# Performance work log

Measured on AMD Instinct MI355X. Metric: run time of the kernel, lower is better.

Reference implementation:

```python
import jax, jax.numpy as jnp
import numpy as np
from jax import lax

# Norse default LIF/LI parameters with dt=0.001
DT_TAU_MEM = 0.1   # dt * tau_mem_inv (1/1e-2)
DT_TAU_SYN = 0.2   # dt * tau_syn_inv (1/5e-3)
V_TH = 0.5
ALPHA = 100.0      # SuperSpike surrogate slope (backward only)

@jax.custom_vjp
def spike(x):
    return (x > 0).astype(x.dtype)

def _spike_fwd(x):
    return (x > 0).astype(x.dtype), x

def _spike_bwd(x, g):
    # SuperSpike surrogate gradient: 1 / (alpha*|x| + 1)^2
    sg = 1.0 / (ALPHA * jnp.abs(x) + 1.0) ** 2
    return (g * sg,)

spike.defvjp(_spike_fwd, _spike_bwd)

def setup_inputs() -> dict:
    key = jax.random.key(0)
    k1, k2, k3 = jax.random.split(key, 3)
    T, B, C, H, W = 64, 512, 1, 28, 28
    IN, HID, OUT = 784, 2048, 10
    x = jax.random.normal(k1, (T, B, C, H, W), dtype=jnp.float32)
    # Kaiming-uniform-ish bias-free Linear weights, torch layout [out, in]
    w1 = jax.random.uniform(k2, (HID, IN), jnp.float32, -1.0, 1.0) / np.sqrt(IN)
    w_out = jax.random.uniform(k3, (OUT, HID), jnp.float32, -1.0, 1.0) / np.sqrt(HID)
    return {"x": x, "w1": w1, "w_out": w_out}

def reference(x, w1, w_out):
    T, B = x.shape[0], x.shape[1]
    HID, OUT = w1.shape[0], w_out.shape[0]
    xf = x.reshape(T, B, -1)  # [T, B, IN]

    def step(carry, xt):
        v1, i1, vo, io = carry
        cur = xt @ w1.T                       # fc1: [B, HID]
        # LIF: decay, threshold/spike/reset, then integrate new input current
        v1_dec = v1 + DT_TAU_MEM * (-v1 + i1)
        i1_dec = i1 * (1.0 - DT_TAU_SYN)
        z = spike(v1_dec - V_TH)
        v1_new = (1.0 - z) * v1_dec           # v_reset = 0
        i1_new = i1_dec + cur
        out_cur = z @ w_out.T                 # fc_out: [B, OUT]
        # LI readout: leaky integration (no spiking)
        vo_new = vo + DT_TAU_MEM * (-vo + io)
        io_new = io * (1.0 - DT_TAU_SYN) + out_cur
        return (v1_new, i1_new, vo_new, io_new), vo_new

    zh = jnp.zeros((B, HID), x.dtype)
    zo = jnp.zeros((B, OUT), x.dtype)
    _, voltages = lax.scan(step, (zh, zh, zo, zo), xf)  # [T, B, OUT]
    return jnp.max(voltages, axis=0)
```

## Files before the change

kernel.cpp:

```cpp
#include <hip/hip_runtime.h>
#include <cstdint>
#include <cstddef>

#define T_STEPS 64
#define BATCH 512
#define IN_F 784
#define NKT 25
#define HID 2048
#define OUT_F 10

#define DEC_V 0.9f
#define DEC_I 0.8f
#define DT_V 0.1f
#define V_TH 0.5f

typedef __attribute__((ext_vector_type(8))) _Float16 f16x8;
typedef __attribute__((ext_vector_type(4))) float f32x4;

__device__ __forceinline__ void load_lds16h(const _Float16* g, _Float16* l) {
  __builtin_amdgcn_global_load_lds(
      (const __attribute__((address_space(1))) void*)g,
      (__attribute__((address_space(3))) void*)l, 16, 0, 0);
}

__global__ __launch_bounds__(256)
void split_frag(const float* __restrict__ src, _Float16* __restrict__ hiT,
                _Float16* __restrict__ loT) {
  __shared__ float xr[16][804];
  const int mt = blockIdx.x;
  for (int i = threadIdx.x; i < 16 * IN_F; i += 256) {
    const int r = i / IN_F, c = i - r * IN_F;
    xr[r][c] = src[(size_t)(mt * 16 + r) * IN_F + c];
  }
  for (int i = threadIdx.x; i < 16 * 16; i += 256)
    xr[i >> 4][IN_F + (i & 15)] = 0.0f;
  __syncthreads();

  const int l = threadIdx.x & 63;
  const int g = threadIdx.x >> 6;
  const int r = l & 15, q = l >> 4;
  for (int kt = g; kt < NKT; kt += 4) {
    const float* s = &xr[r][kt * 32 + q * 8];
    f16x8 h, lo;
#pragma unroll
    for (int j = 0; j < 8; ++j) {
      const float v = s[j];
      const _Float16 hh = (_Float16)v;
      h[j] = hh;
      lo[j] = (_Float16)(v - (float)hh);
    }
    const size_t off = ((size_t)mt * NKT + kt) * 512 + l * 8;
    *(f16x8*)&hiT[off] = h;
    *(f16x8*)&loT[off] = lo;
  }
}

__global__ __launch_bounds__(256, 2)
void gemm_fc1(const _Float16* __restrict__ AhT, const _Float16* __restrict__ AlT,
              const _Float16* __restrict__ WhT, const _Float16* __restrict__ WlT,
              float* __restrict__ C) {
  __shared__ _Float16 __attribute__((aligned(16))) sAh[8 * 512];
  __shared__ _Float16 __attribute__((aligned(16))) sAl[8 * 512];
  __shared__ _Float16 __attribute__((aligned(16))) sWh[16 * 512];
  __shared__ _Float16 __attribute__((aligned(16))) sWl[16 * 512];

  const int tid = threadIdx.x;
  const int lane = tid & 63;
  const int wv = tid >> 6;
  const int bmT = blockIdx.y * 8;
  const int bnT = blockIdx.x * 16;

  const int wrT = (wv >> 1) * 4;
  const int wcT = (wv & 1) * 8;
  const int col = lane & 15;
  const int quad = lane >> 4;

  f32x4 acc[4][8] = {};

  for (int kt = 0; kt < NKT; ++kt) {
    __syncthreads();
#pragma unroll
    for (int j = 0; j < 2; ++j) {
      const int t = wv * 2 + j;
      const size_t go = ((size_t)(bmT + t) * NKT + kt) * 512 + lane * 8;
      load_lds16h(AhT + go, sAh + t * 512);
      load_lds16h(AlT + go, sAl + t * 512);
    }
#pragma unroll
    for (int j = 0; j < 4; ++j) {
      const int t = wv * 4 + j;
      const size_t go = ((size_t)(bnT + t) * NKT + kt) * 512 + lane * 8;
      load_lds16h(WhT + go, sWh + t * 512);
      load_lds16h(WlT + go, sWl + t * 512);
    }
    __syncthreads();

    f16x8 fah[4], fal[4];
#pragma unroll
    for (int i = 0; i < 4; ++i) {
      fah[i] = *(const f16x8*)&sAh[(wrT + i) * 512 + lane * 8];
      fal[i] = *(const f16x8*)&sAl[(wrT + i) * 512 + lane * 8];
    }
#pragma unroll
    for (int ni = 0; ni < 8; ++ni) {
      const f16x8 fwh = *(const f16x8*)&sWh[(wcT + ni) * 512 + lane * 8];
      const f16x8 fwl = *(const f16x8*)&sWl[(wcT + ni) * 512 + lane * 8];
#pragma unroll
      for (int mi = 0; mi < 4; ++mi) {
        acc[mi][ni] = __builtin_amdgcn_mfma_f32_16x16x32_f16(fah[mi], fwh, acc[mi][ni], 0, 0, 0);
        acc[mi][ni] = __builtin_amdgcn_mfma_f32_16x16x32_f16(fah[mi], fwl, acc[mi][ni], 0, 0, 0);
        acc[mi][ni] = __builtin_amdgcn_mfma_f32_16x16x32_f16(fal[mi], fwh, acc[mi][ni], 0, 0, 0);
      }
    }
  }

  const int rowb = blockIdx.y * 128 + (wv >> 1) * 64;
  const int colb = blockIdx.x * 256 + (wv & 1) * 128;
#pragma unroll
  for (int mi = 0; mi < 4; ++mi)
#pragma unroll
    for (int ni = 0; ni < 8; ++ni)
#pragma unroll
      for (int r = 0; r < 4; ++r)
        C[(size_t)(rowb + mi * 16 + quad * 4 + r) * HID + colb + ni * 16 + col] =
            acc[mi][ni][r];
}

__global__ __launch_bounds__(256)
void lif_out(const float* __restrict__ cur, const float* __restrict__ wo,
             float* __restrict__ v1, float* __restrict__ i1,
             float* __restrict__ outP, int tc, int t0) {
  __shared__ _Float16 zL[T_STEPS][264];
  __shared__ _Float16 wT[16][264];

  const int tid = threadIdx.x;
  const int hc = blockIdx.x;
  const int b = blockIdx.y;
  const int hb = hc * 256;

  for (int i = tid; i < 16 * 256; i += 256) {
    const int n = i >> 8, k = i & 255;
    wT[n][k] = (n < OUT_F) ? (_Float16)wo[(size_t)n * HID + hb + k] : (_Float16)0.f;
  }

  const int sidx = b * HID + hb + tid;
  float v = v1[sidx];
  float ci = i1[sidx];
#pragma unroll 4
  for (int t = 0; t < tc; ++t) {
    const float c = cur[(size_t)t * (BATCH * HID) + sidx];
    const float vd = DEC_V * v + DT_V * ci;
    const float z = (vd > V_TH) ? 1.0f : 0.0f;
    v = (1.0f - z) * vd;
    ci = DEC_I * ci + c;
    zL[t][tid] = (_Float16)z;
  }
  v1[sidx] = v;
  i1[sidx] = ci;
  __syncthreads();

  const int wv = tid >> 6;
  const int lane = tid & 63;
  const int col = lane & 15;
  const int quad = lane >> 4;
  f32x4 acc = {};
  const _Float16* za = &zL[wv * 16 + col][0];
  const _Float16* wb = &wT[col][0];
#pragma unroll
  for (int ks = 0; ks < 8; ++ks) {
    f16x8 a = *(const f16x8*)(za + ks * 32 + quad * 8);
    f16x8 bb = *(const f16x8*)(wb + ks * 32 + quad * 8);
    acc = __builtin_amdgcn_mfma_f32_16x16x32_f16(a, bb, acc, 0, 0, 0);
  }
  if (col < OUT_F) {
#pragma unroll
    for (int r = 0; r < 4; ++r) {
      const int t = wv * 16 + quad * 4 + r;
      if (t < tc)
        outP[(((size_t)hc * T_STEPS + (t0 + t)) * BATCH + b) * OUT_F + col] = acc[r];
    }
  }
}

__global__ __launch_bounds__(256)
void li_scan(const float* __restrict__ outP, float* __restrict__ out) {
  const int idx = blockIdx.x * 256 + threadIdx.x;
  if (idx >= BATCH * OUT_F) return;
  float vo = 0.f, io = 0.f, vmax = 0.f;
  for (int t = 0; t < T_STEPS; ++t) {
    float oc = 0.f;
#pragma unroll
    for (int hc = 0; hc < 8; ++hc)
      oc += outP[((size_t)hc * T_STEPS + t) * (BATCH * OUT_F) + idx];
    const float von = DEC_V * vo + DT_V * io;
    io = DEC_I * io + oc;
    vo = von;
    vmax = fmaxf(vmax, von);
  }
  out[idx] = vmax;
}

__global__ void zero_state(float* __restrict__ p, int n) {
  int i = blockIdx.x * 256 + threadIdx.x;
  if (i < n) p[i] = 0.0f;
}

extern "C" void kernel_launch(void* const* d_in, const int* in_sizes, int n_in,
                              void* d_out, int out_size, void* d_ws, size_t ws_size,
                              hipStream_t stream) {
  const float* x  = (const float*)d_in[0];
  const float* w1 = (const float*)d_in[1];
  const float* wo = (const float*)d_in[2];
  float* out = (float*)d_out;

  const size_t BH = (size_t)BATCH * HID;
  const size_t WT_HALVES = (size_t)(HID / 16) * NKT * 512;

  float* v1 = (float*)d_ws;
  float* i1 = v1 + BH;
  float* outP = i1 + BH;
  _Float16* WhT = (_Float16*)(outP + (size_t)8 * T_STEPS * BATCH * OUT_F);
  _Float16* WlT = WhT + WT_HALVES;
  char* chunk0 = (char*)(WlT + WT_HALVES);

  const size_t base_bytes = (size_t)(chunk0 - (char*)d_ws);
  const size_t per_step = BH * 4 + (size_t)2 * 32 * NKT * 512 * 2;
  int Tc = T_STEPS;
  while (Tc > 1 && base_bytes + (size_t)Tc * per_step > ws_size) Tc >>= 1;

  float* cur = (float*)chunk0;
  _Float16* AhT = (_Float16*)(cur + (size_t)Tc * BH);
  _Float16* AlT = AhT + (size_t)Tc * 32 * NKT * 512;

  split_frag<<<HID / 16, 256, 0, stream>>>(w1, WhT, WlT);
  zero_state<<<(int)((2 * BH + 255) / 256), 256, 0, stream>>>(v1, (int)(2 * BH));

  for (int t0 = 0; t0 < T_STEPS; t0 += Tc) {
    const int tc = (T_STEPS - t0 < Tc) ? (T_STEPS - t0) : Tc;
    const int nrows = tc * BATCH;
    split_frag<<<nrows / 16, 256, 0, stream>>>(x + (size_t)t0 * BATCH * IN_F, AhT, AlT);
    dim3 grid(HID / 256, nrows / 128);
    gemm_fc1<<<grid, 256, 0, stream>>>(AhT, AlT, WhT, WlT, cur);
    dim3 lgrid(HID / 256, BATCH);
    lif_out<<<lgrid, 256, 0, stream>>>(cur, wo, v1, i1, outP, tc, t0);
  }
  li_scan<<<(BATCH * OUT_F + 255) / 256, 256, 0, stream>>>(outP, out);
}
```

Measured before the change: 592.2 us.

## Double-buffer A tiles, read W fragments directly from global, swizzle block order

The fc1 GEMM now double-buffers the activation tiles in LDS and prefetches the next k-slice while computing, which removes one barrier per iteration. Weight fragments are no longer staged in LDS; each wave loads them straight from global memory, which relies on cache hits for reuse across blocks. Block IDs are remapped with a swizzle so that blocks sharing rows or columns run closer together, aiming for better L2 locality. The cost is exposed global-load latency for W in the inner loop. The loop-end barrier still keeps each prefetch from overwriting a buffer that is being read.

```diff
diff --git a/kernel.cpp b/kernel.cpp
--- a/kernel.cpp
+++ b/kernel.cpp
@@ -59,16 +59,22 @@
 void gemm_fc1(const _Float16* __restrict__ AhT, const _Float16* __restrict__ AlT,
               const _Float16* __restrict__ WhT, const _Float16* __restrict__ WlT,
               float* __restrict__ C) {
-  __shared__ _Float16 __attribute__((aligned(16))) sAh[8 * 512];
-  __shared__ _Float16 __attribute__((aligned(16))) sAl[8 * 512];
-  __shared__ _Float16 __attribute__((aligned(16))) sWh[16 * 512];
-  __shared__ _Float16 __attribute__((aligned(16))) sWl[16 * 512];
+  __shared__ _Float16 __attribute__((aligned(16))) sAh[2][8 * 512];
+  __shared__ _Float16 __attribute__((aligned(16))) sAl[2][8 * 512];
 
   const int tid = threadIdx.x;
   const int lane = tid & 63;
   const int wv = tid >> 6;
-  const int bmT = blockIdx.y * 8;
-  const int bnT = blockIdx.x * 16;
+
+  const int nwg = gridDim.x * gridDim.y;
+  const int bid = blockIdx.y * gridDim.x + blockIdx.x;
+  const int q = nwg >> 3;
+  const int swz = (bid & 7) * q + (bid >> 3);
+  const int bx = swz & 7;
+  const int by = swz >> 3;
+
+  const int bmT = by * 8;
+  const int bnT = bx * 16;
 
   const int wrT = (wv >> 1) * 4;
   const int wcT = (wv & 1) * 8;
@@ -77,34 +83,40 @@
 
   f32x4 acc[4][8] = {};
 
+#pragma unroll
+  for (int j = 0; j < 2; ++j) {
+    const int t = wv * 2 + j;
+    const size_t go = ((size_t)(bmT + t) * NKT + 0) * 512 + lane * 8;
+    load_lds16h(AhT + go, &sAh[0][t * 512]);
+    load_lds16h(AlT + go, &sAl[0][t * 512]);
+  }
+  __syncthreads();
+
   for (int kt = 0; kt < NKT; ++kt) {
-    __syncthreads();
-#pragma unroll
-    for (int j = 0; j < 2; ++j) {
-      const int t = wv * 2 + j;
-      const size_t go = ((size_t)(bmT + t) * NKT + kt) * 512 + lane * 8;
-      load_lds16h(AhT + go, sAh + t * 512);
-      load_lds16h(AlT + go, sAl + t * 512);
-    }
-#pragma unroll
-    for (int j = 0; j < 4; ++j) {
-      const int t = wv * 4 + j;
-      const size_t go = ((size_t)(bnT + t) * NKT + kt) * 512 + lane * 8;
-      load_lds16h(WhT + go, sWh + t * 512);
-      load_lds16h(WlT + go, sWl + t * 512);
-    }
-    __syncthreads();
+    const int cur = kt & 1;
+    if (kt + 1 < NKT) {
+#pragma unroll
+      for (int j = 0; j < 2; ++j) {
+        const int t = wv * 2 + j;
+        const size_t go = ((size_t)(bmT + t) * NKT + (kt + 1)) * 512 + lane * 8;
+        load_lds16h(AhT + go, &sAh[cur ^ 1][t * 512]);
+        load_lds16h(AlT + go, &sAl[cur ^ 1][t * 512]);
+      }
+    }
 
     f16x8 fah[4], fal[4];
 #pragma unroll
     for (int i = 0; i < 4; ++i) {
-      fah[i] = *(const f16x8*)&sAh[(wrT + i) * 512 + lane * 8];
-      fal[i] = *(const f16x8*)&sAl[(wrT + i) * 512 + lane * 8];
-    }
+      fah[i] = *(const f16x8*)&sAh[cur][(wrT + i) * 512 + lane * 8];
+      fal[i] = *(const f16x8*)&sAl[cur][(wrT + i) * 512 + lane * 8];
+    }
+
+    const size_t wbase = ((size_t)(bnT + wcT) * NKT + kt) * 512 + lane * 8;
 #pragma unroll
     for (int ni = 0; ni < 8; ++ni) {
-      const f16x8 fwh = *(const f16x8*)&sWh[(wcT + ni) * 512 + lane * 8];
-      const f16x8 fwl = *(const f16x8*)&sWl[(wcT + ni) * 512 + lane * 8];
+      const size_t wo = wbase + (size_t)ni * ((size_t)NKT * 512);
+      const f16x8 fwh = *(const f16x8*)&WhT[wo];
+      const f16x8 fwl = *(const f16x8*)&WlT[wo];
 #pragma unroll
       for (int mi = 0; mi < 4; ++mi) {
         acc[mi][ni] = __builtin_amdgcn_mfma_f32_16x16x32_f16(fah[mi], fwh, acc[mi][ni], 0, 0, 0);
@@ -112,10 +124,11 @@
         acc[mi][ni] = __builtin_amdgcn_mfma_f32_16x16x32_f16(fal[mi], fwh, acc[mi][ni], 0, 0, 0);
       }
     }
-  }
-
-  const int rowb = blockIdx.y * 128 + (wv >> 1) * 64;
-  const int colb = blockIdx.x * 256 + (wv & 1) * 128;
+    __syncthreads();
+  }
+
+  const int rowb = by * 128 + (wv >> 1) * 64;
+  const int colb = bx * 256 + (wv & 1) * 128;
 #pragma unroll
   for (int mi = 0; mi < 4; ++mi)
 #pragma unroll
```

After: 679.1 us. 1.15x slower.

## Shrink fc1 GEMM tile to 128x128, raise occupancy, swizzle block order

Applied to the files above, without the earlier changes.

The fc1 split-fp16 GEMM tile drops from 128x256 to 128x128, halving the accumulator registers and W shared-memory buffers so the launch bound can allow five workgroups per CU instead of two. A block-index swizzle spreads consecutive workgroup IDs across eight groups, aiming to improve L2 locality and balance across XCDs. The output store loop is reordered row-major. Smaller tiles reload A twice as often per output, so global and LDS traffic per FLOP rises in exchange for latency hiding.

```diff
diff --git a/kernel.cpp b/kernel.cpp
--- a/kernel.cpp
+++ b/kernel.cpp
@@ -55,75 +55,80 @@
   }
 }
 
-__global__ __launch_bounds__(256, 2)
+__global__ __launch_bounds__(256, 5)
 void gemm_fc1(const _Float16* __restrict__ AhT, const _Float16* __restrict__ AlT,
               const _Float16* __restrict__ WhT, const _Float16* __restrict__ WlT,
               float* __restrict__ C) {
   __shared__ _Float16 __attribute__((aligned(16))) sAh[8 * 512];
   __shared__ _Float16 __attribute__((aligned(16))) sAl[8 * 512];
-  __shared__ _Float16 __attribute__((aligned(16))) sWh[16 * 512];
-  __shared__ _Float16 __attribute__((aligned(16))) sWl[16 * 512];
+  __shared__ _Float16 __attribute__((aligned(16))) sWh[8 * 512];
+  __shared__ _Float16 __attribute__((aligned(16))) sWl[8 * 512];
 
   const int tid = threadIdx.x;
   const int lane = tid & 63;
   const int wv = tid >> 6;
-  const int bmT = blockIdx.y * 8;
-  const int bnT = blockIdx.x * 16;
-
-  const int wrT = (wv >> 1) * 4;
-  const int wcT = (wv & 1) * 8;
+
+  const int nwg = gridDim.x * gridDim.y;
+  const int bid = blockIdx.y * gridDim.x + blockIdx.x;
+  const int q = nwg >> 3;
+  const int swz = (bid & 7) * q + (bid >> 3);
+  const int bx = swz & 15;
+  const int by = swz >> 4;
+
+  const int bmT = by * 8;
+  const int bnT = bx * 8;
+
+  const int wr = wv >> 1;
+  const int wc = wv & 1;
   const int col = lane & 15;
   const int quad = lane >> 4;
 
-  f32x4 acc[4][8] = {};
+  f32x4 acc[4][4] = {};
 
   for (int kt = 0; kt < NKT; ++kt) {
     __syncthreads();
 #pragma unroll
     for (int j = 0; j < 2; ++j) {
       const int t = wv * 2 + j;
-      const size_t go = ((size_t)(bmT + t) * NKT + kt) * 512 + lane * 8;
-      load_lds16h(AhT + go, sAh + t * 512);
-      load_lds16h(AlT + go, sAl + t * 512);
-    }
-#pragma unroll
-    for (int j = 0; j < 4; ++j) {
-      const int t = wv * 4 + j;
-      const size_t go = ((size_t)(bnT + t) * NKT + kt) * 512 + lane * 8;
-      load_lds16h(WhT + go, sWh + t * 512);
-      load_lds16h(WlT + go, sWl + t * 512);
+      const size_t ga = ((size_t)(bmT + t) * NKT + kt) * 512 + lane * 8;
+      load_lds16h(AhT + ga, &sAh[t * 512]);
+      load_lds16h(AlT + ga, &sAl[t * 512]);
+      const size_t gw = ((size_t)(bnT + t) * NKT + kt) * 512 + lane * 8;
+      load_lds16h(WhT + gw, &sWh[t * 512]);
+      load_lds16h(WlT + gw, &sWl[t * 512]);
     }
     __syncthreads();
 
     f16x8 fah[4], fal[4];
 #pragma unroll
     for (int i = 0; i < 4; ++i) {
-      fah[i] = *(const f16x8*)&sAh[(wrT + i) * 512 + lane * 8];
-      fal[i] = *(const f16x8*)&sAl[(wrT + i) * 512 + lane * 8];
-    }
-#pragma unroll
-    for (int ni = 0; ni < 8; ++ni) {
-      const f16x8 fwh = *(const f16x8*)&sWh[(wcT + ni) * 512 + lane * 8];
-      const f16x8 fwl = *(const f16x8*)&sWl[(wcT + ni) * 512 + lane * 8];
+      fah[i] = *(const f16x8*)&sAh[(wr * 4 + i) * 512 + lane * 8];
+      fal[i] = *(const f16x8*)&sAl[(wr * 4 + i) * 512 + lane * 8];
+    }
+#pragma unroll
+    for (int nj = 0; nj < 4; ++nj) {
+      const f16x8 fwh = *(const f16x8*)&sWh[(wc * 4 + nj) * 512 + lane * 8];
+      const f16x8 fwl = *(const f16x8*)&sWl[(wc * 4 + nj) * 512 + lane * 8];
 #pragma unroll
       for (int mi = 0; mi < 4; ++mi) {
-        acc[mi][ni] = __builtin_amdgcn_mfma_f32_16x16x32_f16(fah[mi], fwh, acc[mi][ni], 0, 0, 0);
-        acc[mi][ni] = __builtin_amdgcn_mfma_f32_16x16x32_f16(fah[mi], fwl, acc[mi][ni], 0, 0, 0);
-        acc[mi][ni] = __builtin_amdgcn_mfma_f32_16x16x32_f16(fal[mi], fwh, acc[mi][ni], 0, 0, 0);
+        acc[mi][nj] = __builtin_amdgcn_mfma_f32_16x16x32_f16(fah[mi], fwh, acc[mi][nj], 0, 0, 0);
+        acc[mi][nj] = __builtin_amdgcn_mfma_f32_16x16x32_f16(fah[mi], fwl, acc[mi][nj], 0, 0, 0);
+        acc[mi][nj] = __builtin_amdgcn_mfma_f32_16x16x32_f16(fal[mi], fwh, acc[mi][nj], 0, 0, 0);
       }
     }
   }
 
-  const int rowb = blockIdx.y * 128 + (wv >> 1) * 64;
-  const int colb = blockIdx.x * 256 + (wv & 1) * 128;
+  const int rowb = by * 128 + wr * 64;
+  const int colb = bx * 128 + wc * 64;
 #pragma unroll
   for (int mi = 0; mi < 4; ++mi)
 #pragma unroll
-    for (int ni = 0; ni < 8; ++ni)
-#pragma unroll
-      for (int r = 0; r < 4; ++r)
-        C[(size_t)(rowb + mi * 16 + quad * 4 + r) * HID + colb + ni * 16 + col] =
-            acc[mi][ni][r];
+    for (int r = 0; r < 4; ++r) {
+      const size_t rowo = (size_t)(rowb + mi * 16 + quad * 4 + r) * HID;
+#pragma unroll
+      for (int nj = 0; nj < 4; ++nj)
+        C[rowo + colb + nj * 16 + col] = acc[mi][nj][r];
+    }
 }
 
 __global__ __launch_bounds__(256)
@@ -239,7 +244,7 @@
     const int tc = (T_STEPS - t0 < Tc) ? (T_STEPS - t0) : Tc;
     const int nrows = tc * BATCH;
     split_frag<<<nrows / 16, 256, 0, stream>>>(x + (size_t)t0 * BATCH * IN_F, AhT, AlT);
-    dim3 grid(HID / 256, nrows / 128);
+    dim3 grid(HID / 128, nrows / 128);
     gemm_fc1<<<grid, 256, 0, stream>>>(AhT, AlT, WhT, WlT, cur);
     dim3 lgrid(HID / 256, BATCH);
     lif_out<<<lgrid, 256, 0, stream>>>(cur, wo, v1, i1, outP, tc, t0);
```

New measurement: 1.391 ms. +134.9%, slower.
